# Optimization experiments

Hardware: AMD Instinct MI355X
Metric: run time of the kernel (lower is better)

The kernel has to match this reference:

```python
import jax, jax.numpy as jnp
import numpy as np

N_EMBED = 384
T_MAX = 256
EPS = 1e-5


def layer_norm(x, gamma, beta):
    mu = jnp.mean(x, axis=-1, keepdims=True)
    var = jnp.mean(jnp.square(x - mu), axis=-1, keepdims=True)
    return (x - mu) * jax.lax.rsqrt(var + EPS) * gamma + beta


def setup_inputs() -> dict:
    key = jax.random.key(0)
    ks = jax.random.split(key, 12)
    B, T, C = 128, 256, N_EMBED
    s = lambda fan_in: 1.0 / np.sqrt(fan_in)
    return {
        "x": jax.random.normal(ks[0], (B, T, C), dtype=jnp.float32),
        "W_attn": jax.random.uniform(ks[1], (C, 3 * C), minval=-s(C), maxval=s(C), dtype=jnp.float32),
        "b_attn": jax.random.uniform(ks[2], (3 * C,), minval=-s(C), maxval=s(C), dtype=jnp.float32),
        "W_proj": jax.random.uniform(ks[3], (C, C), minval=-s(C), maxval=s(C), dtype=jnp.float32),
        "b_proj": jax.random.uniform(ks[4], (C,), minval=-s(C), maxval=s(C), dtype=jnp.float32),
        "ln1_g": jnp.ones((C,), jnp.float32),
        "ln1_b": jnp.zeros((C,), jnp.float32),
        "ln2_g": jnp.ones((C,), jnp.float32),
        "ln2_b": jnp.zeros((C,), jnp.float32),
        "W1": jax.random.uniform(ks[5], (C, 4 * C), minval=-s(C), maxval=s(C), dtype=jnp.float32),
        "b1": jax.random.uniform(ks[6], (4 * C,), minval=-s(C), maxval=s(C), dtype=jnp.float32),
        "W2": jax.random.uniform(ks[7], (4 * C, C), minval=-s(4 * C), maxval=s(4 * C), dtype=jnp.float32),
        "b2": jax.random.uniform(ks[8], (4 * C,)[:1] and (C,), minval=-s(4 * C), maxval=s(4 * C), dtype=jnp.float32),
    }


def reference(x, W_attn, b_attn, W_proj, b_proj, ln1_g, ln1_b, ln2_g, ln2_b, W1, b1, W2, b2):
    B, T, C = x.shape
    # --- pre-LN single-head causal self-attention ---
    h = layer_norm(x, ln1_g, ln1_b)
    qkv = h @ W_attn + b_attn                      # [B,T,3C]
    q, k, v = jnp.split(qkv, 3, axis=-1)           # each [B,T,C]
    att = jnp.einsum('btc,bsc->bts', q, k) * (1.0 / jnp.sqrt(jnp.float32(C)))
    causal = jnp.tril(jnp.ones((T, T), bool))
    att = jnp.where(causal, att, -jnp.inf)
    att = jax.nn.softmax(att, axis=-1)             # dropout is identity (eval)
    y = jnp.einsum('bts,bsc->btc', att, v)
    x = x + (y @ W_proj + b_proj)
    # --- pre-LN MLP ---
    h2 = layer_norm(x, ln2_g, ln2_b)
    x = x + (jax.nn.relu(h2 @ W1 + b1) @ W2 + b2)
    return x
```

## Files before the change

kernel.cpp:

```cpp
#include <hip/hip_runtime.h>
#include <hip/hip_bf16.h>

#define C_EMB 384
#define T_SEQ 256
#define B_BATCH 128
#define M_ROWS (B_BATCH * T_SEQ)
#define QKV_LD 1152
#define BK 64

typedef __bf16 bf16_8 __attribute__((ext_vector_type(8)));
typedef float f32x4 __attribute__((ext_vector_type(4)));

__device__ __forceinline__ void load16_lds(const __bf16* g, __bf16* l) {
    __builtin_amdgcn_global_load_lds(
        (const __attribute__((address_space(1))) unsigned int*)g,
        (__attribute__((address_space(3))) unsigned int*)l, 16, 0, 0);
}

__global__ __launch_bounds__(256) void cast_all_kernel(const float* __restrict__ Wa,
                                                       const float* __restrict__ Wp,
                                                       const float* __restrict__ W1,
                                                       const float* __restrict__ W2,
                                                       __bf16* __restrict__ Wa_t,
                                                       __bf16* __restrict__ Wp_t,
                                                       __bf16* __restrict__ W1_t,
                                                       __bf16* __restrict__ W2_t) {
    int bid = blockIdx.x;
    const float* W; __bf16* Wt; int K, N, tx_n;
    if (bid < 432)      { W = Wa; Wt = Wa_t; K = 384;  N = 1152; tx_n = 36; }
    else if (bid < 576) { bid -= 432; W = Wp; Wt = Wp_t; K = 384;  N = 384;  tx_n = 12; }
    else if (bid < 1152){ bid -= 576; W = W1; Wt = W1_t; K = 384;  N = 1536; tx_n = 48; }
    else                { bid -= 1152; W = W2; Wt = W2_t; K = 1536; N = 384;  tx_n = 12; }
    int n0 = (bid % tx_n) * 32, k0 = (bid / tx_n) * 32;

    __shared__ float t[32][33];
    int tx = threadIdx.x & 31, ty = threadIdx.x >> 5;
#pragma unroll
    for (int i = 0; i < 4; ++i)
        t[ty + i * 8][tx] = W[(size_t)(k0 + ty + i * 8) * N + n0 + tx];
    __syncthreads();
#pragma unroll
    for (int i = 0; i < 4; ++i) {
        int n = ty + i * 8;
        Wt[(size_t)(n0 + n) * K + k0 + tx] = (__bf16)t[tx][n];
    }
}

__global__ __launch_bounds__(384) void ln_kernel(const float* __restrict__ x,
                                                 const float* __restrict__ g,
                                                 const float* __restrict__ bta,
                                                 __bf16* __restrict__ out) {
    int row = blockIdx.x;
    int c = threadIdx.x;
    float v = x[(size_t)row * C_EMB + c];

    __shared__ float red[6];
    float s = v;
#pragma unroll
    for (int o = 32; o; o >>= 1) s += __shfl_down(s, o);
    if ((c & 63) == 0) red[c >> 6] = s;
    __syncthreads();
    float mu = (red[0] + red[1] + red[2] + red[3] + red[4] + red[5]) * (1.0f / C_EMB);

    float d = v - mu;
    float s2 = d * d;
#pragma unroll
    for (int o = 32; o; o >>= 1) s2 += __shfl_down(s2, o);
    __syncthreads();
    if ((c & 63) == 0) red[c >> 6] = s2;
    __syncthreads();
    float var = (red[0] + red[1] + red[2] + red[3] + red[4] + red[5]) * (1.0f / C_EMB);

    out[(size_t)row * C_EMB + c] = (__bf16)(d * rsqrtf(var + 1e-5f) * g[c] + bta[c]);
}

template <int TM, bool RELU, bool RESID, bool OUT_BF16>
__global__ __launch_bounds__(256) void mfma_gemm(const __bf16* __restrict__ A, int lda,
                                                 const __bf16* __restrict__ Bt, int ldb,
                                                 const float* __restrict__ bias,
                                                 const float* __restrict__ resid,
                                                 void* __restrict__ out_,
                                                 int N, int K) {
    constexpr int MI = TM / 32;
    constexpr int WROWS = TM / 2;
    __shared__ __align__(16) __bf16 As[2 * TM * 32];
    __shared__ __align__(16) __bf16 Bs[2 * 128 * 32];

    int tid = threadIdx.x;
    int wave = tid >> 6, lane = tid & 63;
    int wr = wave >> 1, wc = wave & 1;
    int quad = lane >> 4, l16 = lane & 15;
    int bm = blockIdx.y * TM, bn = blockIdx.x * 128;
    int lrow = lane >> 2, lcol = (lane & 3) * 8;

    f32x4 acc[MI][4] = {};

    for (int k0 = 0; k0 < K; k0 += BK) {
        const __bf16* Ab = A + (size_t)bm * lda + k0;
        const __bf16* Bb = Bt + (size_t)bn * ldb + k0;
#pragma unroll
        for (int p = 0; p < 2; ++p) {
#pragma unroll
            for (int i = 0; i < TM / 64; ++i) {
                int r0 = (i * 4 + wave) * 16;
                load16_lds(Ab + (size_t)(r0 + lrow) * lda + p * 32 + lcol,
                           &As[p * TM * 32 + r0 * 32]);
            }
#pragma unroll
            for (int i = 0; i < 2; ++i) {
                int r0 = (i * 4 + wave) * 16;
                load16_lds(Bb + (size_t)(r0 + lrow) * ldb + p * 32 + lcol,
                           &Bs[p * 128 * 32 + r0 * 32]);
            }
        }
        __syncthreads();

        bf16_8 af[MI][2], bf[4][2];
#pragma unroll
        for (int p = 0; p < 2; ++p) {
#pragma unroll
            for (int i = 0; i < MI; ++i)
                af[i][p] = *reinterpret_cast<const bf16_8*>(
                    &As[p * TM * 32 + (wr * WROWS + i * 16 + l16) * 32 + quad * 8]);
#pragma unroll
            for (int j = 0; j < 4; ++j)
                bf[j][p] = *reinterpret_cast<const bf16_8*>(
                    &Bs[p * 128 * 32 + (wc * 64 + j * 16 + l16) * 32 + quad * 8]);
        }
#pragma unroll
        for (int i = 0; i < MI; ++i)
#pragma unroll
            for (int j = 0; j < 4; ++j) {
                acc[i][j] = __builtin_amdgcn_mfma_f32_16x16x32_bf16(af[i][0], bf[j][0], acc[i][j], 0, 0, 0);
                acc[i][j] = __builtin_amdgcn_mfma_f32_16x16x32_bf16(af[i][1], bf[j][1], acc[i][j], 0, 0, 0);
            }
        __syncthreads();
    }

#pragma unroll
    for (int i = 0; i < MI; ++i) {
#pragma unroll
        for (int r = 0; r < 4; ++r) {
            int m = bm + wr * WROWS + i * 16 + quad * 4 + r;
#pragma unroll
            for (int j = 0; j < 4; ++j) {
                int n = bn + wc * 64 + j * 16 + l16;
                float v = acc[i][j][r] + bias[n];
                if (RELU) v = fmaxf(v, 0.0f);
                if (RESID) v += resid[(size_t)m * N + n];
                if (OUT_BF16)
                    ((__bf16*)out_)[(size_t)m * N + n] = (__bf16)v;
                else
                    ((float*)out_)[(size_t)m * N + n] = v;
            }
        }
    }
}

__global__ __launch_bounds__(256, 2) void ff2_kernel(const __bf16* __restrict__ A,
                                                     const __bf16* __restrict__ Bt,
                                                     const float* __restrict__ bias,
                                                     float* __restrict__ out) {
    __shared__ __align__(16) __bf16 At[64 * 64];
    __shared__ __align__(16) __bf16 Bs[384 * 64];

    int tid = threadIdx.x;
    int wave = tid >> 6, lane = tid & 63;
    int wr = wave >> 1, wc = wave & 1;
    int quad = lane >> 4, l16 = lane & 15;
    int bm = blockIdx.x * 64;
    int srow = lane >> 3;
    int sunit = (lane & 7) ^ srow;

    f32x4 acc[2][12] = {};

    for (int k0 = 0; k0 < 1536; k0 += BK) {
        __syncthreads();
        {
            const __bf16* asrc = A + (size_t)(bm + srow) * 1536 + k0 + sunit * 8;
#pragma unroll
            for (int t = 0; t < 2; ++t) {
                int g = t * 4 + wave;
                load16_lds(asrc + (size_t)(g * 8) * 1536, &At[g * 8 * 64]);
            }
            const __bf16* bsrc = Bt + (size_t)srow * 1536 + k0 + sunit * 8;
#pragma unroll
            for (int t = 0; t < 12; ++t) {
                int g = t * 4 + wave;
                load16_lds(bsrc + (size_t)(g * 8) * 1536, &Bs[g * 8 * 64]);
            }
        }
        __syncthreads();

        bf16_8 af[2][2];
#pragma unroll
        for (int p = 0; p < 2; ++p)
#pragma unroll
            for (int i = 0; i < 2; ++i) {
                int row = wr * 32 + i * 16 + l16;
                int u = (p * 4 + quad) ^ (row & 7);
                af[i][p] = *reinterpret_cast<const bf16_8*>(&At[row * 64 + u * 8]);
            }
#pragma unroll
        for (int p = 0; p < 2; ++p)
#pragma unroll
            for (int j = 0; j < 12; ++j) {
                int row = wc * 192 + j * 16 + l16;
                int u = (p * 4 + quad) ^ (row & 7);
                bf16_8 bf = *reinterpret_cast<const bf16_8*>(&Bs[row * 64 + u * 8]);
                acc[0][j] = __builtin_amdgcn_mfma_f32_16x16x32_bf16(af[0][p], bf, acc[0][j], 0, 0, 0);
                acc[1][j] = __builtin_amdgcn_mfma_f32_16x16x32_bf16(af[1][p], bf, acc[1][j], 0, 0, 0);
            }
    }

#pragma unroll
    for (int i = 0; i < 2; ++i)
#pragma unroll
        for (int r = 0; r < 4; ++r) {
            int m = bm + wr * 32 + i * 16 + quad * 4 + r;
#pragma unroll
            for (int j = 0; j < 12; ++j) {
                int n = wc * 192 + j * 16 + l16;
                float* o = &out[(size_t)m * C_EMB + n];
                *o = *o + acc[i][j][r] + bias[n];
            }
        }
}

__global__ __launch_bounds__(256) void proj_ln_kernel(const __bf16* __restrict__ A,
                                                      const __bf16* __restrict__ Bt,
                                                      const float* __restrict__ bias,
                                                      const float* __restrict__ resid,
                                                      const float* __restrict__ lng,
                                                      const float* __restrict__ lnb,
                                                      float* __restrict__ out,
                                                      __bf16* __restrict__ h) {
    __shared__ __align__(16) __bf16 As[2 * 64 * 32];
    __shared__ __align__(16) __bf16 Bs[2 * 384 * 32];
    __shared__ float red[2][2][64];

    int tid = threadIdx.x;
    int wave = tid >> 6, lane = tid & 63;
    int wr = wave >> 1, wc = wave & 1;
    int quad = lane >> 4, l16 = lane & 15;
    int bm = blockIdx.x * 64;
    int lrow = lane >> 2, lcol = (lane & 3) * 8;

    f32x4 acc[2][12] = {};

    for (int k0 = 0; k0 < C_EMB; k0 += BK) {
        const __bf16* Ab = A + (size_t)bm * C_EMB + k0;
        const __bf16* Bb = Bt + k0;
#pragma unroll
        for (int p = 0; p < 2; ++p) {
            {
                int r0 = wave * 16;
                load16_lds(Ab + (size_t)(r0 + lrow) * C_EMB + p * 32 + lcol,
                           &As[p * 64 * 32 + r0 * 32]);
            }
#pragma unroll
            for (int i = 0; i < 6; ++i) {
                int r0 = (i * 4 + wave) * 16;
                load16_lds(Bb + (size_t)(r0 + lrow) * C_EMB + p * 32 + lcol,
                           &Bs[p * 384 * 32 + r0 * 32]);
            }
        }
        __syncthreads();

        bf16_8 af[2][2], bf[12][2];
#pragma unroll
        for (int p = 0; p < 2; ++p) {
#pragma unroll
            for (int i = 0; i < 2; ++i)
                af[i][p] = *reinterpret_cast<const bf16_8*>(
                    &As[p * 64 * 32 + (wr * 32 + i * 16 + l16) * 32 + quad * 8]);
#pragma unroll
            for (int j = 0; j < 12; ++j)
                bf[j][p] = *reinterpret_cast<const bf16_8*>(
                    &Bs[p * 384 * 32 + (wc * 192 + j * 16 + l16) * 32 + quad * 8]);
        }
#pragma unroll
        for (int i = 0; i < 2; ++i)
#pragma unroll
            for (int j = 0; j < 12; ++j) {
                acc[i][j] = __builtin_amdgcn_mfma_f32_16x16x32_bf16(af[i][0], bf[j][0], acc[i][j], 0, 0, 0);
                acc[i][j] = __builtin_amdgcn_mfma_f32_16x16x32_bf16(af[i][1], bf[j][1], acc[i][j], 0, 0, 0);
            }
        __syncthreads();
    }

    float bia[12], gg[12], bb[12];
#pragma unroll
    for (int j = 0; j < 12; ++j) {
        int n = wc * 192 + j * 16 + l16;
        bia[j] = bias[n];
        gg[j] = lng[n];
        bb[j] = lnb[n];
    }

#pragma unroll
    for (int i = 0; i < 2; ++i)
#pragma unroll
        for (int r = 0; r < 4; ++r) {
            int rloc = wr * 32 + i * 16 + quad * 4 + r;
            int m = bm + rloc;
            float s = 0.0f, s2 = 0.0f;
#pragma unroll
            for (int j = 0; j < 12; ++j) {
                int n = wc * 192 + j * 16 + l16;
                float v = acc[i][j][r] + bia[j] + resid[(size_t)m * C_EMB + n];
                acc[i][j][r] = v;
                s += v;
                s2 += v * v;
            }
#pragma unroll
            for (int o = 8; o; o >>= 1) {
                s += __shfl_xor(s, o);
                s2 += __shfl_xor(s2, o);
            }
            if (l16 == 0) {
                red[0][wc][rloc] = s;
                red[1][wc][rloc] = s2;
            }
        }
    __syncthreads();

#pragma unroll
    for (int i = 0; i < 2; ++i)
#pragma unroll
        for (int r = 0; r < 4; ++r) {
            int rloc = wr * 32 + i * 16 + quad * 4 + r;
            int m = bm + rloc;
            float mu  = (red[0][0][rloc] + red[0][1][rloc]) * (1.0f / C_EMB);
            float ex2 = (red[1][0][rloc] + red[1][1][rloc]) * (1.0f / C_EMB);
            float rstd = rsqrtf(ex2 - mu * mu + 1e-5f);
#pragma unroll
            for (int j = 0; j < 12; ++j) {
                int n = wc * 192 + j * 16 + l16;
                float v = acc[i][j][r];
                out[(size_t)m * C_EMB + n] = v;
                h[(size_t)m * C_EMB + n] = (__bf16)((v - mu) * rstd * gg[j] + bb[j]);
            }
        }
}

__global__ __launch_bounds__(256) void vt_kernel(const __bf16* __restrict__ qkv,
                                                 __bf16* __restrict__ Vt) {
    __shared__ __align__(16) __bf16 t[32][72];
    int b = blockIdx.z, c0 = blockIdx.x * 64, s0 = blockIdx.y * 32;
    int tid = threadIdx.x;

    int tx = tid & 7, ty = tid >> 3;
    const __bf16* src = qkv + ((size_t)b * T_SEQ + s0 + ty) * QKV_LD + 768 + c0 + tx * 8;
    *reinterpret_cast<float4*>(&t[ty][tx * 8]) = *reinterpret_cast<const float4*>(src);
    __syncthreads();

    int sx = tid & 3, cy = tid >> 2;
    __align__(16) __bf16 tmp[8];
#pragma unroll
    for (int j = 0; j < 8; ++j) tmp[j] = t[sx * 8 + j][cy];
    *reinterpret_cast<float4*>(&Vt[((size_t)b * C_EMB + c0 + cy) * T_SEQ + s0 + sx * 8]) =
        *reinterpret_cast<float4*>(tmp);
}

__global__ __launch_bounds__(256) void qks_mfma(const __bf16* __restrict__ qkv,
                                                __bf16* __restrict__ P) {
    int b = blockIdx.y;
    int bx = blockIdx.x;
    int bm = bx * 128;
    int ntiles = bx + 1;
    const __bf16* Ab0 = qkv + (size_t)b * T_SEQ * QKV_LD;
    const __bf16* Bb0 = Ab0 + 384;

    __shared__ __align__(16) __bf16 As[2 * 128 * 32];
    __shared__ __align__(16) __bf16 Bs[2 * 128 * 32];
    __shared__ float red[2][2][128];

    int tid = threadIdx.x;
    int wave = tid >> 6, lane = tid & 63;
    int wr = wave >> 1, wc = wave & 1;
    int quad = lane >> 4, l16 = lane & 15;
    int lrow = lane >> 2, lcol = (lane & 3) * 8;

    f32x4 acc[2][4][4] = {};

#pragma unroll
    for (int nt = 0; nt < 2; ++nt) {
        if (nt < ntiles) {
            int bn = nt * 128;
            for (int k0 = 0; k0 < C_EMB; k0 += BK) {
                const __bf16* Ab = Ab0 + (size_t)bm * QKV_LD + k0;
                const __bf16* Bb = Bb0 + (size_t)bn * QKV_LD + k0;
#pragma unroll
                for (int p = 0; p < 2; ++p)
#pragma unroll
                    for (int i = 0; i < 2; ++i) {
                        int r0 = (i * 4 + wave) * 16;
                        load16_lds(Ab + (size_t)(r0 + lrow) * QKV_LD + p * 32 + lcol,
                                   &As[p * 128 * 32 + r0 * 32]);
                        load16_lds(Bb + (size_t)(r0 + lrow) * QKV_LD + p * 32 + lcol,
                                   &Bs[p * 128 * 32 + r0 * 32]);
                    }
                __syncthreads();

                bf16_8 af[4][2], bf[4][2];
#pragma unroll
                for (int p = 0; p < 2; ++p)
#pragma unroll
                    for (int i = 0; i < 4; ++i) {
                        af[i][p] = *reinterpret_cast<const bf16_8*>(
                            &As[p * 128 * 32 + (wr * 64 + i * 16 + l16) * 32 + quad * 8]);
                        bf[i][p] = *reinterpret_cast<const bf16_8*>(
                            &Bs[p * 128 * 32 + (wc * 64 + i * 16 + l16) * 32 + quad * 8]);
                    }
#pragma unroll
                for (int i = 0; i < 4; ++i)
#pragma unroll
                    for (int j = 0; j < 4; ++j) {
                        acc[nt][i][j] = __builtin_amdgcn_mfma_f32_16x16x32_bf16(af[i][0], bf[j][0], acc[nt][i][j], 0, 0, 0);
                        acc[nt][i][j] = __builtin_amdgcn_mfma_f32_16x16x32_bf16(af[i][1], bf[j][1], acc[nt][i][j], 0, 0, 0);
                    }
                __syncthreads();
            }
        }
    }

    const float scale = 0.05103103630798288f;

#pragma unroll
    for (int i = 0; i < 4; ++i)
#pragma unroll
        for (int r = 0; r < 4; ++r) {
            int rloc = wr * 64 + i * 16 + quad * 4 + r;
            int t = bm + rloc;
            float m = -INFINITY;
#pragma unroll
            for (int nt = 0; nt < 2; ++nt)
#pragma unroll
                for (int j = 0; j < 4; ++j) {
                    int n = nt * 128 + wc * 64 + j * 16 + l16;
                    bool ok = (nt < ntiles) && (n <= t);
                    float v = acc[nt][i][j][r] * scale;
                    m = fmaxf(m, ok ? v : -INFINITY);
                }
#pragma unroll
            for (int o = 8; o; o >>= 1) m = fmaxf(m, __shfl_xor(m, o));
            if (l16 == 0) red[0][wc][rloc] = m;
        }
    __syncthreads();

#pragma unroll
    for (int i = 0; i < 4; ++i)
#pragma unroll
        for (int r = 0; r < 4; ++r) {
            int rloc = wr * 64 + i * 16 + quad * 4 + r;
            int t = bm + rloc;
            float M = fmaxf(red[0][0][rloc], red[0][1][rloc]);
            float s = 0.0f;
#pragma unroll
            for (int nt = 0; nt < 2; ++nt)
#pragma unroll
                for (int j = 0; j < 4; ++j) {
                    int n = nt * 128 + wc * 64 + j * 16 + l16;
                    bool ok = (nt < ntiles) && (n <= t);
                    float p = ok ? __expf(acc[nt][i][j][r] * scale - M) : 0.0f;
                    acc[nt][i][j][r] = p;
                    s += p;
                }
#pragma unroll
            for (int o = 8; o; o >>= 1) s += __shfl_xor(s, o);
            if (l16 == 0) red[1][wc][rloc] = s;
        }
    __syncthreads();

    __bf16* Pb_ = P + (size_t)b * T_SEQ * T_SEQ;
#pragma unroll
    for (int i = 0; i < 4; ++i)
#pragma unroll
        for (int r = 0; r < 4; ++r) {
            int rloc = wr * 64 + i * 16 + quad * 4 + r;
            float inv = 1.0f / (red[1][0][rloc] + red[1][1][rloc]);
#pragma unroll
            for (int nt = 0; nt < 2; ++nt)
                if (nt < ntiles)
#pragma unroll
                    for (int j = 0; j < 4; ++j) {
                        int n = nt * 128 + wc * 64 + j * 16 + l16;
                        Pb_[(size_t)(bm + rloc) * T_SEQ + n] = (__bf16)(acc[nt][i][j][r] * inv);
                    }
        }
}

__global__ __launch_bounds__(256) void pv_mfma(const __bf16* __restrict__ P,
                                               const __bf16* __restrict__ Vt,
                                               __bf16* __restrict__ y) {
    int b = blockIdx.z;
    int bm = blockIdx.y * 128, bn = blockIdx.x * 128;
    const __bf16* Ab0 = P + (size_t)b * T_SEQ * T_SEQ;
    const __bf16* Bb0 = Vt + (size_t)b * C_EMB * T_SEQ;

    __shared__ __align__(16) __bf16 As[2 * 128 * 32];
    __shared__ __align__(16) __bf16 Bs[2 * 128 * 32];

    int tid = threadIdx.x;
    int wave = tid >> 6, lane = tid & 63;
    int wr = wave >> 1, wc = wave & 1;
    int quad = lane >> 4, l16 = lane & 15;
    int lrow = lane >> 2, lcol = (lane & 3) * 8;

    f32x4 acc[4][4] = {};

    int kmax = bm + 128;
    for (int k0 = 0; k0 < kmax; k0 += BK) {
        const __bf16* Ab = Ab0 + (size_t)bm * T_SEQ + k0;
        const __bf16* Bb = Bb0 + (size_t)bn * T_SEQ + k0;
#pragma unroll
        for (int p = 0; p < 2; ++p)
#pragma unroll
            for (int i = 0; i < 2; ++i) {
                int r0 = (i * 4 + wave) * 16;
                load16_lds(Ab + (size_t)(r0 + lrow) * T_SEQ + p * 32 + lcol,
                           &As[p * 128 * 32 + r0 * 32]);
                load16_lds(Bb + (size_t)(r0 + lrow) * T_SEQ + p * 32 + lcol,
                           &Bs[p * 128 * 32 + r0 * 32]);
            }
        __syncthreads();

        bf16_8 af[4][2], bf[4][2];
#pragma unroll
        for (int p = 0; p < 2; ++p)
#pragma unroll
            for (int i = 0; i < 4; ++i) {
                af[i][p] = *reinterpret_cast<const bf16_8*>(
                    &As[p * 128 * 32 + (wr * 64 + i * 16 + l16) * 32 + quad * 8]);
                bf[i][p] = *reinterpret_cast<const bf16_8*>(
                    &Bs[p * 128 * 32 + (wc * 64 + i * 16 + l16) * 32 + quad * 8]);
            }
#pragma unroll
        for (int i = 0; i < 4; ++i)
#pragma unroll
            for (int j = 0; j < 4; ++j) {
                acc[i][j] = __builtin_amdgcn_mfma_f32_16x16x32_bf16(af[i][0], bf[j][0], acc[i][j], 0, 0, 0);
                acc[i][j] = __builtin_amdgcn_mfma_f32_16x16x32_bf16(af[i][1], bf[j][1], acc[i][j], 0, 0, 0);
            }
        __syncthreads();
    }

#pragma unroll
    for (int i = 0; i < 4; ++i) {
#pragma unroll
        for (int r = 0; r < 4; ++r) {
            int m = bm + wr * 64 + i * 16 + quad * 4 + r;
#pragma unroll
            for (int j = 0; j < 4; ++j) {
                int n = bn + wc * 64 + j * 16 + l16;
                y[((size_t)b * T_SEQ + m) * C_EMB + n] = (__bf16)acc[i][j][r];
            }
        }
    }
}

extern "C" void kernel_launch(void* const* d_in, const int* in_sizes, int n_in,
                              void* d_out, int out_size, void* d_ws, size_t ws_size,
                              hipStream_t stream) {
    const float* x      = (const float*)d_in[0];
    const float* W_attn = (const float*)d_in[1];
    const float* b_attn = (const float*)d_in[2];
    const float* W_proj = (const float*)d_in[3];
    const float* b_proj = (const float*)d_in[4];
    const float* ln1_g  = (const float*)d_in[5];
    const float* ln1_b  = (const float*)d_in[6];
    const float* ln2_g  = (const float*)d_in[7];
    const float* ln2_b  = (const float*)d_in[8];
    const float* W1     = (const float*)d_in[9];
    const float* b1     = (const float*)d_in[10];
    const float* W2     = (const float*)d_in[11];
    const float* b2     = (const float*)d_in[12];
    float* out = (float*)d_out;

    __bf16* Wattn_t = (__bf16*)d_ws;
    __bf16* Wproj_t = Wattn_t + (size_t)1152 * 384;
    __bf16* W1_t    = Wproj_t + (size_t)384 * 384;
    __bf16* W2_t    = W1_t + (size_t)1536 * 384;
    __bf16* h       = W2_t + (size_t)384 * 1536;
    __bf16* yb      = h + (size_t)M_ROWS * 384;
    __bf16* qkv     = yb + (size_t)M_ROWS * 384;
    float*  S       = (float*)(qkv + (size_t)M_ROWS * QKV_LD);
    __bf16* Pb      = (__bf16*)(S + (size_t)B_BATCH * T_SEQ * T_SEQ);
    __bf16* Vt      = Pb + (size_t)B_BATCH * T_SEQ * T_SEQ;
    __bf16* ff      = qkv;

    cast_all_kernel<<<1728, 256, 0, stream>>>(W_attn, W_proj, W1, W2,
                                              Wattn_t, Wproj_t, W1_t, W2_t);

    ln_kernel<<<M_ROWS, 384, 0, stream>>>(x, ln1_g, ln1_b, h);
    mfma_gemm<128, false, false, true><<<dim3(1152 / 128, M_ROWS / 128), 256, 0, stream>>>(
        h, 384, Wattn_t, 384, b_attn, nullptr, qkv, 1152, 384);
    vt_kernel<<<dim3(C_EMB / 64, T_SEQ / 32, B_BATCH), 256, 0, stream>>>(qkv, Vt);
    qks_mfma<<<dim3(2, B_BATCH), 256, 0, stream>>>(qkv, Pb);
    pv_mfma<<<dim3(C_EMB / 128, T_SEQ / 128, B_BATCH), 256, 0, stream>>>(Pb, Vt, yb);
    proj_ln_kernel<<<M_ROWS / 64, 256, 0, stream>>>(yb, Wproj_t, b_proj, x,
                                                    ln2_g, ln2_b, out, h);
    mfma_gemm<128, true, false, true><<<dim3(1536 / 128, M_ROWS / 128), 256, 0, stream>>>(
        h, 384, W1_t, 384, b1, nullptr, ff, 1536, 384);
    ff2_kernel<<<M_ROWS / 64, 256, 0, stream>>>(ff, W2_t, b2, out);
}
```

Measured before the change: 491.8 us.

## Double-buffer LDS and double the row tile in the FF2 GEMM

```diff
diff --git a/kernel.cpp b/kernel.cpp
--- a/kernel.cpp
+++ b/kernel.cpp
@@ -157,40 +157,48 @@
     }
 }
 
-__global__ __launch_bounds__(256, 2) void ff2_kernel(const __bf16* __restrict__ A,
+__global__ __launch_bounds__(512, 1) void ff2_kernel(const __bf16* __restrict__ A,
                                                      const __bf16* __restrict__ Bt,
                                                      const float* __restrict__ bias,
                                                      float* __restrict__ out) {
-    __shared__ __align__(16) __bf16 At[64 * 64];
-    __shared__ __align__(16) __bf16 Bs[384 * 64];
+    __shared__ __align__(16) __bf16 At[2][128 * 64];
+    __shared__ __align__(16) __bf16 Bs[2][384 * 64];
 
     int tid = threadIdx.x;
     int wave = tid >> 6, lane = tid & 63;
     int wr = wave >> 1, wc = wave & 1;
     int quad = lane >> 4, l16 = lane & 15;
-    int bm = blockIdx.x * 64;
+    int bm = blockIdx.x * 128;
     int srow = lane >> 3;
     int sunit = (lane & 7) ^ srow;
 
+    const __bf16* asrc0 = A + (size_t)(bm + srow) * 1536 + sunit * 8;
+    const __bf16* bsrc0 = Bt + (size_t)srow * 1536 + sunit * 8;
+
+    auto stage = [&](int buf, int k0) {
+#pragma unroll
+        for (int t = 0; t < 2; ++t) {
+            int g = t * 8 + wave;
+            load16_lds(asrc0 + (size_t)(g * 8) * 1536 + k0, &At[buf][g * 8 * 64]);
+        }
+#pragma unroll
+        for (int t = 0; t < 6; ++t) {
+            int g = t * 8 + wave;
+            load16_lds(bsrc0 + (size_t)(g * 8) * 1536 + k0, &Bs[buf][g * 8 * 64]);
+        }
+    };
+
     f32x4 acc[2][12] = {};
 
-    for (int k0 = 0; k0 < 1536; k0 += BK) {
-        __syncthreads();
-        {
-            const __bf16* asrc = A + (size_t)(bm + srow) * 1536 + k0 + sunit * 8;
-#pragma unroll
-            for (int t = 0; t < 2; ++t) {
-                int g = t * 4 + wave;
-                load16_lds(asrc + (size_t)(g * 8) * 1536, &At[g * 8 * 64]);
-            }
-            const __bf16* bsrc = Bt + (size_t)srow * 1536 + k0 + sunit * 8;
-#pragma unroll
-            for (int t = 0; t < 12; ++t) {
-                int g = t * 4 + wave;
-                load16_lds(bsrc + (size_t)(g * 8) * 1536, &Bs[g * 8 * 64]);
-            }
-        }
-        __syncthreads();
+    stage(0, 0);
+    asm volatile("s_waitcnt vmcnt(0)" ::: "memory");
+    __builtin_amdgcn_sched_barrier(0);
+    __builtin_amdgcn_s_barrier();
+
+#pragma unroll 2
+    for (int kt = 0; kt < 24; ++kt) {
+        int cur = kt & 1;
+        if (kt < 23) stage(cur ^ 1, (kt + 1) * BK);
 
         bf16_8 af[2][2];
 #pragma unroll
@@ -199,7 +207,7 @@
             for (int i = 0; i < 2; ++i) {
                 int row = wr * 32 + i * 16 + l16;
                 int u = (p * 4 + quad) ^ (row & 7);
-                af[i][p] = *reinterpret_cast<const bf16_8*>(&At[row * 64 + u * 8]);
+                af[i][p] = *reinterpret_cast<const bf16_8*>(&At[cur][row * 64 + u * 8]);
             }
 #pragma unroll
         for (int p = 0; p < 2; ++p)
@@ -207,10 +215,14 @@
             for (int j = 0; j < 12; ++j) {
                 int row = wc * 192 + j * 16 + l16;
                 int u = (p * 4 + quad) ^ (row & 7);
-                bf16_8 bf = *reinterpret_cast<const bf16_8*>(&Bs[row * 64 + u * 8]);
+                bf16_8 bf = *reinterpret_cast<const bf16_8*>(&Bs[cur][row * 64 + u * 8]);
                 acc[0][j] = __builtin_amdgcn_mfma_f32_16x16x32_bf16(af[0][p], bf, acc[0][j], 0, 0, 0);
                 acc[1][j] = __builtin_amdgcn_mfma_f32_16x16x32_bf16(af[1][p], bf, acc[1][j], 0, 0, 0);
             }
+
+        asm volatile("s_waitcnt vmcnt(0)" ::: "memory");
+        __builtin_amdgcn_sched_barrier(0);
+        __builtin_amdgcn_s_barrier();
     }
 
 #pragma unroll
@@ -603,5 +615,5 @@
                                                     ln2_g, ln2_b, out, h);
     mfma_gemm<128, true, false, true><<<dim3(1536 / 128, M_ROWS / 128), 256, 0, stream>>>(
         h, 384, W1_t, 384, b1, nullptr, ff, 1536, 384);
-    ff2_kernel<<<M_ROWS / 64, 256, 0, stream>>>(ff, W2_t, b2, out);
-}
+    ff2_kernel<<<M_ROWS / 128, 512, 0, stream>>>(ff, W2_t, b2, out);
+}
```

Measured after the change: 450.5 us. 8.4% less time.
